# Optimization experiments

Hardware: AMD Instinct MI355X
Metric: run time of the kernel (lower is better)

The kernel has to match this reference:

```python
import jax, jax.numpy as jnp
import numpy as np


def setup_inputs() -> dict:
    key = jax.random.key(0)
    k1, k2, k3 = jax.random.split(key, 3)
    B, C, H, W = 8, 256, 64, 64
    x = jax.random.normal(k1, (B, C, H, W), dtype=jnp.float32)
    mask = (jax.random.uniform(k2, (B, 1, H, W)) < 0.5).astype(jnp.float32)
    # Conv1d(2C, C, kernel_size=1) == matmul with weight (C, 2C) + bias (C,)
    Wc = jax.random.normal(k3, (C, 2 * C), dtype=jnp.float32) * 0.02
    bc = jnp.zeros((C,), dtype=jnp.float32)
    return {"x": x, "mask": mask, "Wc": Wc, "bc": bc}


def reference(x, mask, Wc, bc):
    B, C, H, W = x.shape
    N = H * W
    EPS = 1e-8
    # mask.detach() + nearest interpolate to x's spatial size (sizes already match)
    m = jax.lax.stop_gradient(mask)
    q = (x * m).reshape(B, C, N)              # masked (foreground) features
    s = (x * (1.0 - m)).reshape(B, C, N)      # support (background) features
    q = q / (jnp.linalg.norm(q, axis=1, keepdims=True) + EPS)
    s = s / (jnp.linalg.norm(s, axis=1, keepdims=True) + EPS)
    # per-batch cosine similarity: (B, N, N)
    sim = jnp.einsum('bcn,bcm->bnm', q, s)
    # top-1 over support dim (k = 1)
    idx = jnp.argmax(sim, axis=2)             # (B, N) selected support index per query pos
    wv = jnp.max(sim, axis=2)                 # (B, N) top-1 similarity value
    fore_wv = jnp.max(sim, axis=1)            # (B, N) top-1 over query dim
    fm = m.reshape(B, N)
    # faithful quirk: validmask = validmask[0, :, 0] keeps only support position 0 -> per-sample scalar
    valid = ((fore_wv[:, 0] > 0.5).astype(x.dtype) * fm[:, 0])[:, None, None]  # (B,1,1)
    # gather selected support features: select[b,c,j] = s[b,c,idx[b,j]]
    select = jnp.take_along_axis(s, idx[:, None, :], axis=2)  # (B, C, N)
    # faithful quirk: with k=1, Softmax(dim=-1) acts over the H*W axis (same per channel)
    w = jax.nn.softmax(wv, axis=-1)           # (B, N)
    fuse = select * w[:, None, :]             # (B, C, N)  (sum over k=1 is identity)
    hybrid = jnp.concatenate([fuse, q], axis=1)               # (B, 2C, N)
    hybrid = jnp.einsum('bin,oi->bon', hybrid, Wc) + bc[None, :, None]  # 1x1 conv
    hybrid = hybrid * valid + q * (1.0 - valid)
    refined = hybrid.reshape(B, C, H, W)
    # attmask holds only the LAST sample's indices (loop variable overwritten)
    attmap = jnp.zeros((B, N), dtype=x.dtype).at[:, idx[-1]].set(1.0)
    attmap = attmap.reshape(B, 1, H, W)
    attmap = jnp.repeat(jnp.repeat(attmap, 8, axis=2), 8, axis=3)  # nearest x8 upsample
    out = refined * m + x * (1.0 - m)
    return out, attmap
```

## Files before the change

### kernel.cpp

```cpp
#include <hip/hip_runtime.h>
#include <cmath>

#define B_ 8
#define C_ 256
#define N_ 4096
#define EPS_ 1e-8f

typedef _Float16 half8 __attribute__((ext_vector_type(8)));
typedef float f32x4 __attribute__((ext_vector_type(4)));
typedef unsigned short ushort8 __attribute__((ext_vector_type(8)));

__device__ __forceinline__ void gload_lds16(const void* g, void* l) {
  __builtin_amdgcn_global_load_lds((const __attribute__((address_space(1))) unsigned int*)g,
                                   (__attribute__((address_space(3))) unsigned int*)l, 16, 0, 0);
}

__device__ __forceinline__ float block_fore(const float* __restrict__ partMax, int b) {
  int l = threadIdx.x & 63;
  float v = partMax[(b << 6) + l];
#pragma unroll
  for (int d = 32; d; d >>= 1) v = fmaxf(v, __shfl_xor(v, d, 64));
  return v;
}

__global__ __launch_bounds__(512) void k_base(const float* __restrict__ x, const float* __restrict__ mask,
                                              float* __restrict__ fq, float* __restrict__ fs,
                                              float* __restrict__ out, float* __restrict__ partMax,
                                              int* __restrict__ mark,
                                              unsigned short* __restrict__ qhi, unsigned short* __restrict__ qlo,
                                              unsigned short* __restrict__ shi, unsigned short* __restrict__ slo) {
  int b = blockIdx.y, n0 = blockIdx.x << 6;
  int t = threadIdx.x;
  int ln = t & 63, cg = t >> 6;
  __shared__ float sred[512];
  __shared__ float s0[256];
  __shared__ float rss[8][64], rdp[8][64];
  __shared__ float scaleS[64], f64q[64], f64s[64];
  __shared__ float bcast[2];
  if (b == 0 && blockIdx.x == 0) {
#pragma unroll
    for (int i = 0; i < 8; ++i) mark[t + (i << 9)] = 0;
  }
  const size_t xbase = ((size_t)b * C_) << 12;
  float xc0 = 0.f;
  if (t < 256) xc0 = x[xbase + ((size_t)t << 12)];
  sred[t] = xc0 * xc0;
  __syncthreads();
  for (int s = 256; s; s >>= 1) { if (t < s) sred[t] += sred[t + s]; __syncthreads(); }
  if (t == 0) { bcast[0] = 1.f / (sqrtf(sred[0]) + EPS_); bcast[1] = mask[b << 12]; }
  __syncthreads();
  if (t < 256) s0[t] = xc0 * ((1.f - bcast[1]) * bcast[0]);
  __syncthreads();
  int n = n0 + ln;
  const float* xp = x + xbase + (((size_t)cg) << 17) + n;
  float xv[32];
  float ss = 0.f, dp = 0.f;
#pragma unroll
  for (int c = 0; c < 32; ++c) {
    float v = xp[(size_t)c << 12];
    xv[c] = v;
    ss += v * v;
    dp += v * s0[(cg << 5) + c];
  }
  rss[cg][ln] = ss; rdp[cg][ln] = dp;
  __syncthreads();
  if (t < 64) {
    float sst = 0.f, dpt = 0.f;
#pragma unroll
    for (int g = 0; g < 8; ++g) { sst += rss[g][t]; dpt += rdp[g][t]; }
    float inv = 1.f / (sqrtf(sst) + EPS_);
    float m = mask[(b << 12) + n0 + t];
    float fqv = m * inv;
    fq[(b << 12) + n0 + t] = fqv;
    fs[(b << 12) + n0 + t] = (1.f - m) * inv;
    scaleS[t] = (m != 0.f) ? inv : 1.f;
    f64q[t] = fqv * 64.0f;
    f64s[t] = (1.f - m) * inv * 64.0f;
    float val = dpt * fqv;
#pragma unroll
    for (int d = 32; d; d >>= 1) val = fmaxf(val, __shfl_xor(val, d, 64));
    if (t == 0) partMax[(b << 6) + blockIdx.x] = val;
  }
  __syncthreads();
  float sc = scaleS[ln];
  float* op = out + xbase + (((size_t)cg) << 17) + n;
#pragma unroll
  for (int c = 0; c < 32; ++c) op[(size_t)c << 12] = xv[c] * sc;
  if (b == B_ - 1) {
    float fqn = f64q[ln], fsn = f64s[ln];
    int swz = (n >> 1) & 3;
    size_t rowbase = ((size_t)n) << 8;
#pragma unroll
    for (int j = 0; j < 4; ++j) {
      ushort8 vqh, vql, vsh, vsl;
#pragma unroll
      for (int i = 0; i < 8; ++i) {
        float xvv = xv[j * 8 + i];
        float qv = xvv * fqn;
        _Float16 qh = (_Float16)qv;
        _Float16 ql = (_Float16)((qv - (float)qh) * 2048.0f);
        float sv = xvv * fsn;
        _Float16 sh = (_Float16)sv;
        _Float16 sl = (_Float16)((sv - (float)sh) * 2048.0f);
        vqh[i] = __builtin_bit_cast(unsigned short, qh);
        vql[i] = __builtin_bit_cast(unsigned short, ql);
        vsh[i] = __builtin_bit_cast(unsigned short, sh);
        vsl[i] = __builtin_bit_cast(unsigned short, sl);
      }
      size_t off = rowbase + ((size_t)cg << 5) + (size_t)((j ^ swz) << 3);
      *reinterpret_cast<ushort8*>(qhi + off) = vqh;
      *reinterpret_cast<ushort8*>(qlo + off) = vql;
      *reinterpret_cast<ushort8*>(shi + off) = vsh;
      *reinterpret_cast<ushort8*>(slo + off) = vsl;
    }
  }
}

__global__ __launch_bounds__(256, 2) void k_sim7(const unsigned short* __restrict__ qhi, const unsigned short* __restrict__ qlo,
                                                 const unsigned short* __restrict__ shi, const unsigned short* __restrict__ slo,
                                                 float* __restrict__ partV, int* __restrict__ partI) {
  int bid = blockIdx.x;
  int xcd = bid & 7;
  int r = bid >> 3;
  int scol = r >> 4;
  int w16 = r & 15;
  int nt = (xcd << 2) + (w16 >> 2);
  int mt = (scol << 2) + (w16 & 3);
  int tid = threadIdx.x;
  int w = tid >> 6, lane = tid & 63;
  int wy = w >> 1, wx = w & 1;
  __shared__ __align__(16) unsigned short smem[2][16384];

  f32x4 acc_h[4][4], acc_c[4][4];
#pragma unroll
  for (int i = 0; i < 4; ++i)
#pragma unroll
    for (int j = 0; j < 4; ++j) {
      acc_h[i][j] = (f32x4){0.f, 0.f, 0.f, 0.f};
      acc_c[i][j] = (f32x4){0.f, 0.f, 0.f, 0.f};
    }

  const unsigned short* gsrc = (w == 0) ? qhi : (w == 1) ? qlo : (w == 2) ? shi : slo;
  int n0 = ((w < 2) ? nt : mt) << 7;
  int lrow = lane >> 2, lch = lane & 3;
  int s = lane >> 4, c16 = lane & 15;

#define STAGE7(buf, kt)                                                                              \
  _Pragma("unroll")                                                                                  \
  for (int seg = 0; seg < 8; ++seg) {                                                                \
    const unsigned short* g = gsrc + (((size_t)(n0 + (seg << 4) + lrow)) << 8) + ((kt) << 5) + (lch << 3); \
    gload_lds16(g, &smem[buf][(w << 12) + (seg << 9)]);                                              \
  }

  STAGE7(0, 0);

  int cur = 0;
  for (int kt = 0; kt < 8; ++kt) {
    if (kt < 7) {
      STAGE7(cur ^ 1, kt + 1);
      asm volatile("s_waitcnt vmcnt(8)" ::: "memory");
    } else {
      asm volatile("s_waitcnt vmcnt(0)" ::: "memory");
    }
    __builtin_amdgcn_s_barrier();
    __builtin_amdgcn_sched_barrier(0);
    const unsigned short* sm = &smem[cur][0];
    half8 ah[4], al[4], bh[4], bl[4];
#pragma unroll
    for (int f = 0; f < 4; ++f) {
      int ra = (wy << 6) + (f << 4) + c16;
      int oa = ra * 32 + ((s ^ ((ra >> 1) & 3)) << 3);
      ah[f] = *reinterpret_cast<const half8*>(&sm[oa]);
      al[f] = *reinterpret_cast<const half8*>(&sm[4096 + oa]);
      int rb = (wx << 6) + (f << 4) + c16;
      int ob = rb * 32 + ((s ^ ((rb >> 1) & 3)) << 3);
      bh[f] = *reinterpret_cast<const half8*>(&sm[8192 + ob]);
      bl[f] = *reinterpret_cast<const half8*>(&sm[12288 + ob]);
    }
#pragma unroll
    for (int fi = 0; fi < 4; ++fi)
#pragma unroll
      for (int fj = 0; fj < 4; ++fj) {
        acc_h[fi][fj] = __builtin_amdgcn_mfma_f32_16x16x32_f16(ah[fi], bh[fj], acc_h[fi][fj], 0, 0, 0);
        acc_c[fi][fj] = __builtin_amdgcn_mfma_f32_16x16x32_f16(ah[fi], bl[fj], acc_c[fi][fj], 0, 0, 0);
        acc_c[fi][fj] = __builtin_amdgcn_mfma_f32_16x16x32_f16(al[fi], bh[fj], acc_c[fi][fj], 0, 0, 0);
      }
    asm volatile("s_waitcnt lgkmcnt(0)" ::: "memory");
    __builtin_amdgcn_s_barrier();
    __builtin_amdgcn_sched_barrier(0);
    cur ^= 1;
  }
#undef STAGE7
  float* redV = reinterpret_cast<float*>(&smem[0][0]);
  int* redI = reinterpret_cast<int*>(&smem[0][512]);
  int g16 = lane >> 4;
#pragma unroll
  for (int fi = 0; fi < 4; ++fi)
#pragma unroll
    for (int r2 = 0; r2 < 4; ++r2) {
      float bv = -INFINITY; int bi = 0x7fffffff;
#pragma unroll
      for (int fj = 0; fj < 4; ++fj) {
        float v = (acc_h[fi][fj][r2] + acc_c[fi][fj][r2] * (1.0f / 2048.0f)) * (1.0f / 4096.0f);
        int colg = (mt << 7) + (wx << 6) + (fj << 4) + c16;
        if (v > bv) { bv = v; bi = colg; }
      }
#pragma unroll
      for (int d = 1; d < 16; d <<= 1) {
        float ov = __shfl_xor(bv, d, 64);
        int oi = __shfl_xor(bi, d, 64);
        if (ov > bv || (ov == bv && oi < bi)) { bv = ov; bi = oi; }
      }
      if (c16 == 0) {
        int row = (wy << 6) + (fi << 4) + (g16 << 2) + r2;
        redV[row * 2 + wx] = bv;
        redI[row * 2 + wx] = bi;
      }
    }
  __syncthreads();
  if (tid < 128) {
    float v0 = redV[tid * 2], v1 = redV[tid * 2 + 1];
    int i0 = redI[tid * 2], i1 = redI[tid * 2 + 1];
    if (v1 > v0 || (v1 == v0 && i1 < i0)) { v0 = v1; i0 = i1; }
    int n = (nt << 7) + tid;
    partV[(((size_t)n) << 5) + mt] = v0;
    partI[(((size_t)n) << 5) + mt] = i0;
  }
}

__global__ __launch_bounds__(256) void k_simL(const float* __restrict__ x, const float* __restrict__ mask,
                                              const float* __restrict__ partMax,
                                              const float* __restrict__ fq, const float* __restrict__ fs,
                                              float* __restrict__ wv, int* __restrict__ idxv) {
  int b = blockIdx.y;
  float fore = block_fore(partMax, b);
  if (!(fore > 0.5f) || mask[b << 12] == 0.f) return;
  int n0 = blockIdx.x << 6;
  int tid = threadIdx.x;
  int tx = tid & 15, ty = tid >> 4;
  int lk = ty, ln4 = tx << 2;

  __shared__ float As[16][68];
  __shared__ float Bs[16][68];
  __shared__ float fqs[64], fss[64];
  __shared__ float rv[64][17];
  __shared__ int ri[64][17];

  if (tid < 64) fqs[tid] = fq[(b << 12) + n0 + tid];

  float bestv[4]; int besti[4];
#pragma unroll
  for (int i = 0; i < 4; ++i) { bestv[i] = -INFINITY; besti[i] = 0; }

  const size_t xb = ((size_t)b * C_) << 12;

  for (int m0 = 0; m0 < N_; m0 += 64) {
    if (tid < 64) fss[tid] = fs[(b << 12) + m0 + tid];
    float cacc[4][4];
#pragma unroll
    for (int i = 0; i < 4; ++i)
#pragma unroll
      for (int j = 0; j < 4; ++j) cacc[i][j] = 0.f;
    __syncthreads();
    for (int kt = 0; kt < C_; kt += 16) {
      float4 va = *reinterpret_cast<const float4*>(x + xb + ((size_t)(kt + lk) << 12) + n0 + ln4);
      float4 vb = *reinterpret_cast<const float4*>(x + xb + ((size_t)(kt + lk) << 12) + m0 + ln4);
      va.x *= fqs[ln4]; va.y *= fqs[ln4 + 1]; va.z *= fqs[ln4 + 2]; va.w *= fqs[ln4 + 3];
      vb.x *= fss[ln4]; vb.y *= fss[ln4 + 1]; vb.z *= fss[ln4 + 2]; vb.w *= fss[ln4 + 3];
      *reinterpret_cast<float4*>(&As[lk][ln4]) = va;
      *reinterpret_cast<float4*>(&Bs[lk][ln4]) = vb;
      __syncthreads();
#pragma unroll
      for (int k = 0; k < 16; ++k) {
        float a0 = As[k][(ty << 2) + 0], a1 = As[k][(ty << 2) + 1], a2 = As[k][(ty << 2) + 2], a3 = As[k][(ty << 2) + 3];
        float b0 = Bs[k][(tx << 2) + 0], b1 = Bs[k][(tx << 2) + 1], b2 = Bs[k][(tx << 2) + 2], b3 = Bs[k][(tx << 2) + 3];
        cacc[0][0] += a0 * b0; cacc[0][1] += a0 * b1; cacc[0][2] += a0 * b2; cacc[0][3] += a0 * b3;
        cacc[1][0] += a1 * b0; cacc[1][1] += a1 * b1; cacc[1][2] += a1 * b2; cacc[1][3] += a1 * b3;
        cacc[2][0] += a2 * b0; cacc[2][1] += a2 * b1; cacc[2][2] += a2 * b2; cacc[2][3] += a2 * b3;
        cacc[3][0] += a3 * b0; cacc[3][1] += a3 * b1; cacc[3][2] += a3 * b2; cacc[3][3] += a3 * b3;
      }
      __syncthreads();
    }
#pragma unroll
    for (int j = 0; j < 4; ++j) {
      int col = m0 + (tx << 2) + j;
#pragma unroll
      for (int i = 0; i < 4; ++i) {
        float v = cacc[i][j];
        if (v > bestv[i]) { bestv[i] = v; besti[i] = col; }
      }
    }
  }
#pragma unroll
  for (int i = 0; i < 4; ++i) { rv[(ty << 2) + i][tx] = bestv[i]; ri[(ty << 2) + i][tx] = besti[i]; }
  __syncthreads();
  if (tid < 64) {
    float bv = rv[tid][0]; int bi = ri[tid][0];
#pragma unroll
    for (int t = 1; t < 16; ++t) {
      float v = rv[tid][t]; int ii = ri[tid][t];
      if (v > bv || (v == bv && ii < bi)) { bv = v; bi = ii; }
    }
    wv[(b << 12) + n0 + tid] = bv;
    idxv[(b << 12) + n0 + tid] = bi;
  }
}

__global__ __launch_bounds__(256) void k_red7m(const float* __restrict__ p7V, const int* __restrict__ p7I,
                                               float* __restrict__ wv, int* __restrict__ idxv,
                                               int* __restrict__ mark) {
  int n = blockIdx.x * 256 + threadIdx.x;
  float bv = -INFINITY; int bi = 0x7fffffff;
#pragma unroll 8
  for (int mtv = 0; mtv < 32; ++mtv) {
    float v = p7V[(((size_t)n) << 5) + mtv];
    int i = p7I[(((size_t)n) << 5) + mtv];
    if (v > bv || (v == bv && i < bi)) { bv = v; bi = i; }
  }
  wv[((B_ - 1) << 12) + n] = bv;
  idxv[((B_ - 1) << 12) + n] = bi;
  mark[bi] = 1;
}

__global__ __launch_bounds__(256) void k_hybrid(const float* __restrict__ x, const float* __restrict__ mask,
                                                const float* __restrict__ partMax,
                                                const float* __restrict__ fq, const float* __restrict__ fs,
                                                const float* __restrict__ Wc, const float* __restrict__ bc,
                                                const int* __restrict__ idxv, const float* __restrict__ wv,
                                                float* __restrict__ out) {
  int b = blockIdx.y;
  float fore = block_fore(partMax, b);
  if (!(fore > 0.5f) || mask[b << 12] == 0.f) return;
  int tid = threadIdx.x;
  __shared__ float red[256];
  float mx = -INFINITY;
  for (int n = tid; n < N_; n += 256) mx = fmaxf(mx, wv[(b << 12) + n]);
  red[tid] = mx; __syncthreads();
  for (int s = 128; s; s >>= 1) { if (tid < s) red[tid] = fmaxf(red[tid], red[tid + s]); __syncthreads(); }
  mx = red[0]; __syncthreads();
  float sm = 0.f;
  for (int n = tid; n < N_; n += 256) sm += expf(wv[(b << 12) + n] - mx);
  red[tid] = sm; __syncthreads();
  for (int s = 128; s; s >>= 1) { if (tid < s) red[tid] += red[tid + s]; __syncthreads(); }
  float den = red[0];

  int n = blockIdx.x * 256 + tid;
  int bn = (b << 12) + n;
  float mn = mask[bn];
  if (mn == 0.f) return;
  int j = idxv[bn];
  float w = expf(wv[bn] - mx) / den;
  float fsj = fs[(b << 12) + j];
  float fqn = fq[bn];
  const float* xb = x + (((size_t)b * C_) << 12);
  for (int o = 0; o < C_; ++o) {
    const float* wr = Wc + o * 2 * C_;
    float a1 = 0.f, a2 = 0.f;
    for (int i = 0; i < C_; ++i) {
      a1 += wr[i] * xb[((size_t)i << 12) + j];
      a2 += wr[C_ + i] * xb[((size_t)i << 12) + n];
    }
    out[((size_t)(b * C_ + o) << 12) + n] = bc[o] + a1 * (fsj * w) + a2 * fqn;
  }
}

__global__ __launch_bounds__(256) void k_att(const int* __restrict__ mark, float* __restrict__ att) {
  int id = blockIdx.x * 256 + threadIdx.x;
  int x8 = (id & 63) << 3;
  int y = (id >> 6) & 511;
  int b = id >> 15;
  float v = mark[((y >> 3) << 6) + (x8 >> 3)] ? 1.f : 0.f;
  float4 vv = make_float4(v, v, v, v);
  float* p = att + (((size_t)b) << 18) + (y << 9) + x8;
  *reinterpret_cast<float4*>(p) = vv;
  *reinterpret_cast<float4*>(p + 4) = vv;
}

extern "C" void kernel_launch(void* const* d_in, const int* in_sizes, int n_in,
                              void* d_out, int out_size, void* d_ws, size_t ws_size,
                              hipStream_t stream) {
  const float* x = (const float*)d_in[0];
  const float* mask = (const float*)d_in[1];
  const float* Wc = (const float*)d_in[2];
  const float* bc = (const float*)d_in[3];
  float* out = (float*)d_out;
  float* att = out + (size_t)B_ * C_ * N_;

  float* wsf = (float*)d_ws;
  float* fq = wsf;
  float* fs = wsf + 32768;
  float* wv = wsf + 65536;
  int* idxv = (int*)(wsf + 98304);
  int* mark = (int*)(wsf + 655392);
  float* partMax = wsf + 659488;
  float* p7V = wsf + 660000;
  int* p7I = (int*)(wsf + 791072);
  unsigned short* qhi = (unsigned short*)(wsf + 922144);
  unsigned short* qlo = (unsigned short*)(wsf + 1446432);
  unsigned short* shi = (unsigned short*)(wsf + 1970720);
  unsigned short* slo = (unsigned short*)(wsf + 2495008);

  k_base<<<dim3(64, B_), 512, 0, stream>>>(x, mask, fq, fs, out, partMax, mark, qhi, qlo, shi, slo);
  k_sim7<<<1024, 256, 0, stream>>>(qhi, qlo, shi, slo, p7V, p7I);
  k_simL<<<dim3(64, B_ - 1), 256, 0, stream>>>(x, mask, partMax, fq, fs, wv, idxv);
  k_red7m<<<16, 256, 0, stream>>>(p7V, p7I, wv, idxv, mark);
  k_hybrid<<<dim3(16, B_), 256, 0, stream>>>(x, mask, partMax, fq, fs, Wc, bc, idxv, wv, out);
  k_att<<<1024, 256, 0, stream>>>(mark, att);
}
```

Before: 74.56 us.

## Compact last-sample similarity GEMM to foreground rows and background columns

Adds a single-block prefix-scan kernel that splits last-sample positions into foreground rows and background columns and writes gather index lists. The last-sample similarity GEMM gathers only nonzero q rows and s columns through these lists and exits early for tiles beyond the counts, so with a half-density mask it does roughly a quarter of the MFMA work. All-zero rows and columns are handled analytically in the reduction, including zero-similarity ties against the first background index. The LDS swizzle moves from the producer's store layout into the gather offsets. The cost is one extra serial launch and indirect loads in the GEMM staging.

```diff
diff --git a/kernel.cpp b/kernel.cpp
--- a/kernel.cpp
+++ b/kernel.cpp
@@ -21,6 +21,60 @@
 #pragma unroll
   for (int d = 32; d; d >>= 1) v = fmaxf(v, __shfl_xor(v, d, 64));
   return v;
+}
+
+__global__ __launch_bounds__(1024) void k_cmp7(const float* __restrict__ mask,
+                                               int* __restrict__ rowsrc, int* __restrict__ rowrank,
+                                               int* __restrict__ colsrc, int* __restrict__ colmapG,
+                                               int* __restrict__ cnt) {
+  int t = threadIdx.x;
+#pragma unroll
+  for (int i = 0; i < 4; ++i) {
+    rowsrc[t + (i << 10)] = 0;
+    colsrc[t + (i << 10)] = 0;
+    colmapG[t + (i << 10)] = 0x3fffffff;
+  }
+  __syncthreads();
+  int n0 = t << 2;
+  int f[4]; int pk = 0;
+#pragma unroll
+  for (int i = 0; i < 4; ++i) {
+    int m = (mask[(7 << 12) + n0 + i] != 0.f) ? 1 : 0;
+    f[i] = m;
+    pk += m ? 1 : (1 << 16);
+  }
+  int incl = pk;
+#pragma unroll
+  for (int d = 1; d < 64; d <<= 1) {
+    int o = __shfl_up(incl, d, 64);
+    if ((t & 63) >= d) incl += o;
+  }
+  __shared__ int wtot[16], wbase[16], stot;
+  if ((t & 63) == 63) wtot[t >> 6] = incl;
+  __syncthreads();
+  if (t < 16) {
+    int s = 0;
+    for (int i = 0; i < t; ++i) s += wtot[i];
+    wbase[t] = s;
+    if (t == 15) stot = s + wtot[15];
+  }
+  __syncthreads();
+  int excl = wbase[t >> 6] + incl - pk;
+  int rslot = excl & 0xffff, cslot = excl >> 16;
+#pragma unroll
+  for (int i = 0; i < 4; ++i) {
+    int n = n0 + i;
+    if (f[i]) { rowsrc[rslot] = n; rowrank[n] = rslot; ++rslot; }
+    else      { rowrank[n] = -1; colsrc[cslot] = n; colmapG[cslot] = n; ++cslot; }
+  }
+  __syncthreads();
+  if (t == 0) {
+    int tot = stot;
+    int nr = tot & 0xffff;
+    cnt[0] = nr;
+    cnt[1] = tot >> 16;
+    cnt[2] = (nr > 0) ? rowsrc[0] : 0x7fffffff;
+  }
 }
 
 __global__ __launch_bounds__(512) void k_base(const float* __restrict__ x, const float* __restrict__ mask,
@@ -88,7 +142,6 @@
   for (int c = 0; c < 32; ++c) op[(size_t)c << 12] = xv[c] * sc;
   if (b == B_ - 1) {
     float fqn = f64q[ln], fsn = f64s[ln];
-    int swz = (n >> 1) & 3;
     size_t rowbase = ((size_t)n) << 8;
 #pragma unroll
     for (int j = 0; j < 4; ++j) {
@@ -107,7 +160,7 @@
         vsh[i] = __builtin_bit_cast(unsigned short, sh);
         vsl[i] = __builtin_bit_cast(unsigned short, sl);
       }
-      size_t off = rowbase + ((size_t)cg << 5) + (size_t)((j ^ swz) << 3);
+      size_t off = rowbase + ((size_t)cg << 5) + ((size_t)j << 3);
       *reinterpret_cast<ushort8*>(qhi + off) = vqh;
       *reinterpret_cast<ushort8*>(qlo + off) = vql;
       *reinterpret_cast<ushort8*>(shi + off) = vsh;
@@ -118,14 +171,13 @@
 
 __global__ __launch_bounds__(256, 2) void k_sim7(const unsigned short* __restrict__ qhi, const unsigned short* __restrict__ qlo,
                                                  const unsigned short* __restrict__ shi, const unsigned short* __restrict__ slo,
+                                                 const int* __restrict__ rowsrc, const int* __restrict__ colsrc,
+                                                 const int* __restrict__ colmapG, const int* __restrict__ cnt,
                                                  float* __restrict__ partV, int* __restrict__ partI) {
+  int nrows = cnt[0], ncols = cnt[1];
   int bid = blockIdx.x;
-  int xcd = bid & 7;
-  int r = bid >> 3;
-  int scol = r >> 4;
-  int w16 = r & 15;
-  int nt = (xcd << 2) + (w16 >> 2);
-  int mt = (scol << 2) + (w16 & 3);
+  int mt = bid & 31, nt = bid >> 5;
+  if ((nt << 7) >= nrows || (mt << 7) >= ncols) return;
   int tid = threadIdx.x;
   int w = tid >> 6, lane = tid & 63;
   int wy = w >> 1, wx = w & 1;
@@ -141,15 +193,21 @@
     }
 
   const unsigned short* gsrc = (w == 0) ? qhi : (w == 1) ? qlo : (w == 2) ? shi : slo;
+  const int* srcmap = (w < 2) ? rowsrc : colsrc;
   int n0 = ((w < 2) ? nt : mt) << 7;
   int lrow = lane >> 2, lch = lane & 3;
+  int chx = (lch ^ ((lrow >> 1) & 3)) << 3;
   int s = lane >> 4, c16 = lane & 15;
-
-#define STAGE7(buf, kt)                                                                              \
-  _Pragma("unroll")                                                                                  \
-  for (int seg = 0; seg < 8; ++seg) {                                                                \
-    const unsigned short* g = gsrc + (((size_t)(n0 + (seg << 4) + lrow)) << 8) + ((kt) << 5) + (lch << 3); \
-    gload_lds16(g, &smem[buf][(w << 12) + (seg << 9)]);                                              \
+  int srco[8];
+#pragma unroll
+  for (int seg = 0; seg < 8; ++seg)
+    srco[seg] = (srcmap[n0 + (seg << 4) + lrow] << 8) + chx;
+
+#define STAGE7(buf, kt)                                                                \
+  _Pragma("unroll")                                                                    \
+  for (int seg = 0; seg < 8; ++seg) {                                                  \
+    const unsigned short* g = gsrc + (size_t)(srco[seg] + ((kt) << 5));                \
+    gload_lds16(g, &smem[buf][(w << 12) + (seg << 9)]);                                \
   }
 
   STAGE7(0, 0);
@@ -191,6 +249,13 @@
     cur ^= 1;
   }
 #undef STAGE7
+  int cg4[4], cok[4];
+#pragma unroll
+  for (int fj = 0; fj < 4; ++fj) {
+    int slotg = (mt << 7) + (wx << 6) + (fj << 4) + c16;
+    cg4[fj] = colmapG[slotg];
+    cok[fj] = slotg < ncols;
+  }
   float* redV = reinterpret_cast<float*>(&smem[0][0]);
   int* redI = reinterpret_cast<int*>(&smem[0][512]);
   int g16 = lane >> 4;
@@ -201,8 +266,9 @@
       float bv = -INFINITY; int bi = 0x7fffffff;
 #pragma unroll
       for (int fj = 0; fj < 4; ++fj) {
-        float v = (acc_h[fi][fj][r2] + acc_c[fi][fj][r2] * (1.0f / 2048.0f)) * (1.0f / 4096.0f);
-        int colg = (mt << 7) + (wx << 6) + (fj << 4) + c16;
+        float v = cok[fj] ? (acc_h[fi][fj][r2] + acc_c[fi][fj][r2] * (1.0f / 2048.0f)) * (1.0f / 4096.0f)
+                          : -INFINITY;
+        int colg = cg4[fj];
         if (v > bv) { bv = v; bi = colg; }
       }
 #pragma unroll
@@ -307,15 +373,27 @@
 }
 
 __global__ __launch_bounds__(256) void k_red7m(const float* __restrict__ p7V, const int* __restrict__ p7I,
+                                               const int* __restrict__ rowrank, const int* __restrict__ cnt,
                                                float* __restrict__ wv, int* __restrict__ idxv,
                                                int* __restrict__ mark) {
   int n = blockIdx.x * 256 + threadIdx.x;
-  float bv = -INFINITY; int bi = 0x7fffffff;
-#pragma unroll 8
-  for (int mtv = 0; mtv < 32; ++mtv) {
-    float v = p7V[(((size_t)n) << 5) + mtv];
-    int i = p7I[(((size_t)n) << 5) + mtv];
-    if (v > bv || (v == bv && i < bi)) { bv = v; bi = i; }
+  int ncols = cnt[1], j0 = cnt[2];
+  int rk = rowrank[n];
+  float bv; int bi;
+  if (rk < 0) {
+    bv = 0.f; bi = 0;
+  } else {
+    bv = -INFINITY; bi = 0x7fffffff;
+    int mtmax = (ncols + 127) >> 7;
+    for (int mt = 0; mt < mtmax; ++mt) {
+      float v = p7V[(((size_t)rk) << 5) + mt];
+      int i = p7I[(((size_t)rk) << 5) + mt];
+      if (v > bv || (v == bv && i < bi)) { bv = v; bi = i; }
+    }
+    if (j0 < N_) {
+      if (0.f > bv) { bv = 0.f; bi = j0; }
+      else if (0.f == bv && j0 < bi) bi = j0;
+    }
   }
   wv[((B_ - 1) << 12) + n] = bv;
   idxv[((B_ - 1) << 12) + n] = bi;
@@ -391,6 +469,11 @@
   float* fs = wsf + 32768;
   float* wv = wsf + 65536;
   int* idxv = (int*)(wsf + 98304);
+  int* rowsrc = (int*)(wsf + 131072);
+  int* rowrank = (int*)(wsf + 135168);
+  int* colsrc = (int*)(wsf + 139264);
+  int* colmapG = (int*)(wsf + 143360);
+  int* cnt = (int*)(wsf + 147456);
   int* mark = (int*)(wsf + 655392);
   float* partMax = wsf + 659488;
   float* p7V = wsf + 660000;
@@ -400,10 +483,11 @@
   unsigned short* shi = (unsigned short*)(wsf + 1970720);
   unsigned short* slo = (unsigned short*)(wsf + 2495008);
 
+  k_cmp7<<<1, 1024, 0, stream>>>(mask, rowsrc, rowrank, colsrc, colmapG, cnt);
   k_base<<<dim3(64, B_), 512, 0, stream>>>(x, mask, fq, fs, out, partMax, mark, qhi, qlo, shi, slo);
-  k_sim7<<<1024, 256, 0, stream>>>(qhi, qlo, shi, slo, p7V, p7I);
+  k_sim7<<<1024, 256, 0, stream>>>(qhi, qlo, shi, slo, rowsrc, colsrc, colmapG, cnt, p7V, p7I);
   k_simL<<<dim3(64, B_ - 1), 256, 0, stream>>>(x, mask, partMax, fq, fs, wv, idxv);
-  k_red7m<<<16, 256, 0, stream>>>(p7V, p7I, wv, idxv, mark);
+  k_red7m<<<16, 256, 0, stream>>>(p7V, p7I, rowrank, cnt, wv, idxv, mark);
   k_hybrid<<<dim3(16, B_), 256, 0, stream>>>(x, mask, partMax, fq, fs, Wc, bc, idxv, wv, out);
   k_att<<<1024, 256, 0, stream>>>(mark, att);
 }
```

Result: faster. 71.94 us (-3.5%).
